# Kernel tuning notes

Measured on AMD Instinct MI355X. Metric: run time of the kernel, lower is better.

## Reference

```python
import jax, jax.numpy as jnp
import numpy as np

N = 100000        # nodes
E = 1600000       # edges (before self loops)
IN_DIM = 128
OUT_DIM = 64
HEADS = 4
CH = OUT_DIM // HEADS   # 16 channels per head
G = 64            # graphs in batch
EPS = 1e-5        # GraphNorm eps
SLOPE = 0.2       # LeakyReLU negative slope (GATv2Conv default)


def setup_inputs() -> dict:
    key = jax.random.key(0)
    ks = jax.random.split(key, 8)
    x = jax.random.normal(ks[0], (N, IN_DIM), dtype=jnp.float32)
    edge_index = jax.random.randint(ks[1], (2, E), 0, N, dtype=jnp.int64)
    batch = jnp.sort(jax.random.randint(ks[2], (N,), 0, G, dtype=jnp.int64))
    s_in = 1.0 / np.sqrt(IN_DIM)
    # GATv2Conv params (share_weights=False): W_l for source, W_r for target
    Wl = jax.random.normal(ks[3], (IN_DIM, HEADS * CH), dtype=jnp.float32) * s_in
    Wr = jax.random.normal(ks[4], (IN_DIM, HEADS * CH), dtype=jnp.float32) * s_in
    att = jax.random.normal(ks[5], (HEADS, CH), dtype=jnp.float32) * (1.0 / np.sqrt(CH))
    conv_bias = jnp.zeros((HEADS * CH,), dtype=jnp.float32)
    # skip Linear
    skip_W = jax.random.normal(ks[6], (IN_DIM, OUT_DIM), dtype=jnp.float32) * s_in
    skip_b = jax.random.normal(ks[7], (OUT_DIM,), dtype=jnp.float32) * s_in
    # GraphNorm params (PyG init: weight=1, bias=0, mean_scale=1)
    ones = jnp.ones((OUT_DIM,), dtype=jnp.float32)
    zeros = jnp.zeros((OUT_DIM,), dtype=jnp.float32)
    return {
        "x": x, "edge_index": edge_index, "batch": batch,
        "Wl": Wl, "Wr": Wr, "att": att, "conv_bias": conv_bias,
        "skip_W": skip_W, "skip_b": skip_b,
        "bn_w": ones, "bn_b": zeros, "bn_ms": ones,
        "sn_w": ones, "sn_b": zeros, "sn_ms": ones,
    }


def _gatv2(x, Wl, Wr, att, bias, src, dst):
    n = x.shape[0]
    xl = (x @ Wl).reshape(n, HEADS, CH)   # source transform (also the message)
    xr = (x @ Wr).reshape(n, HEADS, CH)   # target transform
    # GATv2: score = a . LeakyReLU(xl[j] + xr[i]) per head
    e = jax.nn.leaky_relu(xl[src] + xr[dst], SLOPE)          # [E,H,C]
    score = jnp.einsum('ehc,hc->eh', e, att)                  # [E,H]
    # segment softmax over edges sharing a target node
    smax = jax.ops.segment_max(score, dst, num_segments=n)    # [N,H]
    ex = jnp.exp(score - smax[dst])
    denom = jax.ops.segment_sum(ex, dst, num_segments=n)
    alpha = ex / denom[dst]                                   # [E,H]
    out = jax.ops.segment_sum(xl[src] * alpha[:, :, None], dst, num_segments=n)
    return out.reshape(n, HEADS * CH) + bias


def _graph_norm(x, w, b, ms, batch):
    cnt = jax.ops.segment_sum(jnp.ones((x.shape[0],), x.dtype), batch, num_segments=G)
    cnt = jnp.maximum(cnt, 1.0)[:, None]
    mean = jax.ops.segment_sum(x, batch, num_segments=G) / cnt
    cen = x - mean[batch] * ms
    var = jax.ops.segment_sum(cen * cen, batch, num_segments=G) / cnt
    inv = jax.lax.rsqrt(var + EPS)
    return w * cen * inv[batch] + b


def reference(x, edge_index, batch, Wl, Wr, att, conv_bias, skip_W, skip_b,
              bn_w, bn_b, bn_ms, sn_w, sn_b, sn_ms):
    n = x.shape[0]
    loop = jnp.arange(n, dtype=edge_index.dtype)  # add_self_loops=True default
    src = jnp.concatenate([edge_index[0], loop])
    dst = jnp.concatenate([edge_index[1], loop])
    x_main = _gatv2(x, Wl, Wr, att, conv_bias, src, dst)
    x_main = _graph_norm(x_main, bn_w, bn_b, bn_ms, batch)
    x_skip = _graph_norm(x @ skip_W + skip_b, sn_w, sn_b, sn_ms, batch)
    return jax.nn.elu(x_main + x_skip)
```

## Files before the change

kernel.cpp:

```cpp
#include <hip/hip_runtime.h>

#define IND 128
#define OUTD 64
#define NG 64
#define NPART 8
#define NSTRIPE 256
#define SLOPE 0.2f
#define EPSV 1e-5f
#define JMASK 131071
#define DEGCAP 48

typedef short bf16x8 __attribute__((ext_vector_type(8)));
typedef float f32x4 __attribute__((ext_vector_type(4)));
typedef float f32x2 __attribute__((ext_vector_type(2)));

__device__ __forceinline__ unsigned bf16rne(float f) {
  unsigned u = __float_as_uint(f);
  return (u + 0x7fffu + ((u >> 16) & 1u)) >> 16;
}
__device__ __forceinline__ unsigned pack2(float a, float b) {
  return bf16rne(a) | (bf16rne(b) << 16);
}
__device__ __forceinline__ unsigned pack2u(unsigned a, unsigned b) {
  return pack2(__uint_as_float(a), __uint_as_float(b));
}

__device__ __forceinline__ void gload_lds16(const void* g, void* l) {
  __builtin_amdgcn_global_load_lds(
      (const __attribute__((address_space(1))) void*)g,
      (__attribute__((address_space(3))) void*)l, 16, 0, 0);
}

__global__ __launch_bounds__(256) void wcvt_kernel(
    const float* __restrict__ Wl, const float* __restrict__ Wr,
    const float* __restrict__ Ws, unsigned short* __restrict__ wt) {
  int i = blockIdx.x * 256 + threadIdx.x;
  if (i >= 3 * 64 * 128) return;
  int k = i & 127, col = (i >> 7) & 63, which = i >> 13;
  const float* W = (which == 0) ? Wl : (which == 1) ? Wr : Ws;
  int row = which * 64 + col;
  int t = row >> 4, m = row & 15;
  int kc = k >> 5, quad = (k >> 3) & 3, j = k & 7;
  int slot = ((t * 4 + kc) * 4 + quad) * 16 + m;
  wt[slot * 8 + j] = (unsigned short)bf16rne(W[k * OUTD + col]);
}

__device__ __forceinline__ void gemm3_body(
    int bx, const float* __restrict__ x, const unsigned short* __restrict__ wt,
    const float* __restrict__ skip_b,
    unsigned* __restrict__ xlb, float* __restrict__ xr, float* __restrict__ xs,
    int n, uint4* ldsx) {
  int tid = threadIdx.x;
  int wave = tid >> 6, lane = tid & 63;
  int m = lane & 15, quad = lane >> 4;

#pragma unroll
  for (int i = 0; i < 8; ++i) {
    int c = i * 256 + tid;
    int row = c >> 5, u = c & 31;
    int us = u ^ (row & 7);
    int growc = min(bx * 64 + row, n - 1);
    gload_lds16(x + (size_t)growc * IND + us * 4, &ldsx[c]);
  }
  __syncthreads();

  int lbase = (wave * 16 + m) * 32;
  int swz = m & 7;
  union { uint4 u; bf16x8 v; } af[4];
#pragma unroll
  for (int kc = 0; kc < 4; ++kc) {
    int u0 = kc * 8 + quad * 2;
    uint4 A0 = ldsx[lbase + (u0 ^ swz)];
    uint4 A1 = ldsx[lbase + ((u0 + 1) ^ swz)];
    af[kc].u = make_uint4(pack2u(A0.x, A0.y), pack2u(A0.z, A0.w),
                          pack2u(A1.x, A1.y), pack2u(A1.z, A1.w));
  }

  f32x4 acc[12] = {};
#pragma unroll
  for (int kc = 0; kc < 4; ++kc) {
#pragma unroll
    for (int t = 0; t < 12; ++t) {
      const bf16x8* bp =
          (const bf16x8*)&wt[(((t * 4 + kc) * 4 + quad) * 16 + m) * 8];
      acc[t] = __builtin_amdgcn_mfma_f32_16x16x32_bf16(af[kc].v, *bp, acc[t], 0, 0, 0);
    }
  }

  float sbv[4];
#pragma unroll
  for (int q = 0; q < 4; ++q) sbv[q] = skip_b[q * 16 + m];

  int orow_base = bx * 64 + wave * 16 + quad * 4;
#pragma unroll
  for (int r = 0; r < 4; ++r) {
    int orow = orow_base + r;
    bool ok = orow < n;
#pragma unroll
    for (int t = 0; t < 4; ++t) {
      float v = acc[t][r];
      float pv = __shfl_xor(v, 1);
      if (ok && !(m & 1))
        xlb[(orow << 5) + t * 8 + (m >> 1)] = pack2(v, pv);
    }
#pragma unroll
    for (int t = 4; t < 8; ++t)
      if (ok) xr[(orow << 6) + (t - 4) * 16 + m] = acc[t][r];
#pragma unroll
    for (int t = 8; t < 12; ++t)
      if (ok) xs[(orow << 6) + (t - 8) * 16 + m] = acc[t][r] + sbv[t - 8];
  }
}

__device__ __forceinline__ void scat1(int d, int s, int lo, int hi,
                                      int* count, int* __restrict__ bucket) {
  if (d >= lo && d < hi) {
    int p = atomicAdd(&count[d], 1);
    if (p < DEGCAP) bucket[d * DEGCAP + p] = s;
  }
}

__device__ __forceinline__ void scatter_body(int r, int stripe,
                                             const int* __restrict__ src,
                                             const int* __restrict__ dst,
                                             int* count, int* __restrict__ bucket,
                                             int E, int n8) {
  int lo = r * n8, hi = lo + n8;
  int per = (((E + NSTRIPE - 1) / NSTRIPE) + 3) & ~3;
  int s0 = stripe * per;
  int s1 = min(E, s0 + per);
  for (int e = s0 + (int)threadIdx.x * 4; e < s1; e += 1024) {
    if (e + 4 <= s1) {
      int4 d4 = *(const int4*)&dst[e];
      int4 s4 = *(const int4*)&src[e];
      scat1(d4.x, s4.x, lo, hi, count, bucket);
      scat1(d4.y, s4.y, lo, hi, count, bucket);
      scat1(d4.z, s4.z, lo, hi, count, bucket);
      scat1(d4.w, s4.w, lo, hi, count, bucket);
    } else {
      for (int q = e; q < s1; ++q)
        scat1(dst[q], src[q], lo, hi, count, bucket);
    }
  }
}

__device__ __forceinline__ void goff_body(int bx, const int* __restrict__ batch,
                                          int* goff, int n) {
  int i = bx * 256 + threadIdx.x;
  if (i >= n) return;
  int b = batch[i];
  int prev = (i == 0) ? -1 : batch[i - 1];
  for (int g = prev + 1; g <= b; ++g) goff[g] = i;
  if (i == n - 1)
    for (int g = b + 1; g <= NG; ++g) goff[g] = n;
}

__global__ __launch_bounds__(256) void mega1_kernel(
    const float* __restrict__ x, const unsigned short* __restrict__ wt,
    const float* __restrict__ skip_b,
    unsigned* __restrict__ xlb, float* __restrict__ xr, float* __restrict__ xs,
    const int* __restrict__ src, const int* __restrict__ dst,
    int* count, int* bucket,
    const int* __restrict__ batch, int* goff,
    int n, int E, int n8, int nbG, int nbB, int SG, int GG) {
  __shared__ uint4 ldsx[2048];
  int group = blockIdx.x >> 3, pos = blockIdx.x & 7;
  int mn = min(SG, GG), m2 = 2 * mn;
  bool isS;
  int sub;
  if (group < m2) { isS = ((group & 1) == 0); sub = group >> 1; }
  else           { isS = (SG > GG);           sub = mn + (group - m2); }
  if (isS) {
    scatter_body(pos, sub, src, dst, count, bucket, E, n8);
  } else {
    int g = sub * 8 + pos;
    if (g < nbG) gemm3_body(g, x, wt, skip_b, xlb, xr, xs, n, ldsx);
    else if (g < nbG + nbB) goff_body(g - nbG, batch, goff, n);
  }
}

__global__ __launch_bounds__(256) void edge_kernel(
    const unsigned* __restrict__ xlb, const float* __restrict__ xr,
    const int* __restrict__ count, const int* __restrict__ bucket,
    const float* __restrict__ att, const float* __restrict__ conv_bias,
    float* __restrict__ out_main, int n) {
  int tid = threadIdx.x;
  int wave = tid >> 6;
  int lane = tid & 63;
  int half = lane >> 5;
  int sub = lane & 31;
  int bx = (int)blockIdx.x;
  int node = bx * 8 + wave * 2 + half;
  bool act = node < n;
  int nodec = min(node, n - 1);
  int base2 = (nodec << 6) | (sub << 1);

  f32x2 xrc = __builtin_nontemporal_load((const f32x2*)&xr[base2]);
  unsigned us = xlb[(nodec << 5) | sub];
  float xs0 = __uint_as_float(us << 16);
  float xs1 = __uint_as_float(us & 0xffff0000u);
  float2 att2 = *(const float2*)&att[sub << 1];

  float t0 = xs0 + xrc.x, t1 = xs1 + xrc.y;
  t0 = fmaxf(t0, SLOPE * t0);
  t1 = fmaxf(t1, SLOPE * t1);
  float s = t0 * att2.x + t1 * att2.y;
  s += __shfl_xor(s, 1);
  s += __shfl_xor(s, 2);
  s += __shfl_xor(s, 4);
  const float sself = s;

  int e0 = nodec * DEGCAP;
  int deg = min(count[nodec], DEGCAP);
  int iters = max(deg, __shfl_xor(deg, 32));

  float denom = 1.f;
  float a0 = xs0, a1 = xs1;
  int i = 0;
  for (; i + 3 < iters; i += 4) {
    float p[4], v0[4], v1[4];
#pragma unroll
    for (int k = 0; k < 4; ++k) {
      bool a = (i + k < deg);
      int e = a ? (e0 + i + k) : e0;
      int j = bucket[e] & JMASK;
      unsigned u = xlb[(j << 5) | sub];
      v0[k] = __uint_as_float(u << 16);
      v1[k] = __uint_as_float(u & 0xffff0000u);
      float tx = v0[k] + xrc.x, ty = v1[k] + xrc.y;
      tx = fmaxf(tx, SLOPE * tx); ty = fmaxf(ty, SLOPE * ty);
      float sc = tx * att2.x + ty * att2.y;
      sc += __shfl_xor(sc, 1);
      sc += __shfl_xor(sc, 2);
      sc += __shfl_xor(sc, 4);
      p[k] = a ? __expf(sc - sself) : 0.f;
    }
#pragma unroll
    for (int k = 0; k < 4; ++k) {
      denom += p[k];
      a0 += p[k] * v0[k];
      a1 += p[k] * v1[k];
    }
  }
  for (; i < iters; ++i) {
    bool a = (i < deg);
    int e = a ? (e0 + i) : e0;
    int j = bucket[e] & JMASK;
    unsigned u = xlb[(j << 5) | sub];
    float v0 = __uint_as_float(u << 16);
    float v1 = __uint_as_float(u & 0xffff0000u);
    float tx = v0 + xrc.x, ty = v1 + xrc.y;
    tx = fmaxf(tx, SLOPE * tx); ty = fmaxf(ty, SLOPE * ty);
    float sc = tx * att2.x + ty * att2.y;
    sc += __shfl_xor(sc, 1);
    sc += __shfl_xor(sc, 2);
    sc += __shfl_xor(sc, 4);
    float p = a ? __expf(sc - sself) : 0.f;
    denom += p;
    a0 += p * v0;
    a1 += p * v1;
  }
  float inv = 1.f / denom;
  float2 cb = *(const float2*)&conv_bias[sub << 1];
  if (act) {
    f32x2 o; o.x = a0 * inv + cb.x; o.y = a1 * inv + cb.y;
    __builtin_nontemporal_store(o, (f32x2*)&out_main[base2]);
  }
}

__global__ __launch_bounds__(256) void stats_part_kernel(
    const float* __restrict__ mainv, const float* __restrict__ xs,
    const int* __restrict__ goff, float* __restrict__ part) {
  int g = blockIdx.x, q = blockIdx.y;
  int start = goff[g], end = goff[g + 1];
  int col = threadIdx.x & 63, grp = threadIdx.x >> 6;
  float s1m = 0.f, s2m = 0.f, s1s = 0.f, s2s = 0.f;
  for (int node = start + q * 4 + grp; node < end; node += 4 * NPART) {
    float vm = __builtin_nontemporal_load(&mainv[(node << 6) | col]);
    float vs = __builtin_nontemporal_load(&xs[(node << 6) | col]);
    s1m += vm; s2m += vm * vm;
    s1s += vs; s2s += vs * vs;
  }
  __shared__ float red[4][4][64];
  red[0][grp][col] = s1m; red[1][grp][col] = s2m;
  red[2][grp][col] = s1s; red[3][grp][col] = s2s;
  __syncthreads();
  if (threadIdx.x < 64) {
    int c = threadIdx.x;
    float* dst = &part[(g * NPART + q) * 256];
#pragma unroll
    for (int st = 0; st < 4; ++st) {
      float s = red[st][0][c] + red[st][1][c] + red[st][2][c] + red[st][3][c];
      dst[st * 64 + c] = s;
    }
  }
}

__global__ void stats_comb_kernel(
    const float* __restrict__ part, const int* __restrict__ goff,
    const float* __restrict__ bn_w, const float* __restrict__ bn_b,
    const float* __restrict__ bn_ms,
    const float* __restrict__ sn_w, const float* __restrict__ sn_b,
    const float* __restrict__ sn_ms,
    float* __restrict__ Am, float* __restrict__ Bm,
    float* __restrict__ As, float* __restrict__ Bs) {
  int g = blockIdx.x;
  int c = threadIdx.x;
  float S1m = 0.f, S2m = 0.f, S1s = 0.f, S2s = 0.f;
  for (int q = 0; q < NPART; ++q) {
    const float* p = &part[(g * NPART + q) * 256];
    S1m += p[c];       S2m += p[64 + c];
    S1s += p[128 + c]; S2s += p[192 + c];
  }
  float cnt = fmaxf((float)(goff[g + 1] - goff[g]), 1.f);
  float meanM = S1m / cnt;
  float aM = meanM * bn_ms[c];
  float varM = S2m / cnt - 2.f * aM * meanM + aM * aM;
  float invM = rsqrtf(varM + EPSV);
  float am = bn_w[c] * invM;
  Am[g * OUTD + c] = am;
  Bm[g * OUTD + c] = bn_b[c] - am * aM;
  float meanS = S1s / cnt;
  float aS = meanS * sn_ms[c];
  float varS = S2s / cnt - 2.f * aS * meanS + aS * aS;
  float invS = rsqrtf(varS + EPSV);
  float as_ = sn_w[c] * invS;
  As[g * OUTD + c] = as_;
  Bs[g * OUTD + c] = sn_b[c] - as_ * aS;
}

__global__ __launch_bounds__(256) void final_kernel(
    const float* __restrict__ xs, const int* __restrict__ batch,
    const float* __restrict__ Am, const float* __restrict__ Bm,
    const float* __restrict__ As, const float* __restrict__ Bs,
    float* out, int n) {
  int idx = blockIdx.x * 256 + threadIdx.x;
  if (idx >= n * 16) return;
  int node = idx >> 4;
  int c4 = (idx & 15) << 2;
  int g = batch[node];
  f32x4 mv = __builtin_nontemporal_load((const f32x4*)&out[idx << 2]);
  f32x4 sv = __builtin_nontemporal_load((const f32x4*)&xs[idx << 2]);
  f32x4 A1 = *(const f32x4*)&Am[g * OUTD + c4];
  f32x4 B1 = *(const f32x4*)&Bm[g * OUTD + c4];
  f32x4 A2 = *(const f32x4*)&As[g * OUTD + c4];
  f32x4 B2 = *(const f32x4*)&Bs[g * OUTD + c4];
  f32x4 v;
  v.x = A1.x * mv.x + B1.x + A2.x * sv.x + B2.x;
  v.y = A1.y * mv.y + B1.y + A2.y * sv.y + B2.y;
  v.z = A1.z * mv.z + B1.z + A2.z * sv.z + B2.z;
  v.w = A1.w * mv.w + B1.w + A2.w * sv.w + B2.w;
  v.x = (v.x > 0.f) ? v.x : (__expf(v.x) - 1.f);
  v.y = (v.y > 0.f) ? v.y : (__expf(v.y) - 1.f);
  v.z = (v.z > 0.f) ? v.z : (__expf(v.z) - 1.f);
  v.w = (v.w > 0.f) ? v.w : (__expf(v.w) - 1.f);
  __builtin_nontemporal_store(v, (f32x4*)&out[idx << 2]);
}

extern "C" void kernel_launch(void* const* d_in, const int* in_sizes, int n_in,
                              void* d_out, int out_size, void* d_ws, size_t ws_size,
                              hipStream_t stream) {
  const float* x        = (const float*)d_in[0];
  const int*   ei       = (const int*)d_in[1];
  const int*   batch    = (const int*)d_in[2];
  const float* Wl       = (const float*)d_in[3];
  const float* Wr       = (const float*)d_in[4];
  const float* att      = (const float*)d_in[5];
  const float* conv_b   = (const float*)d_in[6];
  const float* skip_W   = (const float*)d_in[7];
  const float* skip_b   = (const float*)d_in[8];
  const float* bn_w     = (const float*)d_in[9];
  const float* bn_b     = (const float*)d_in[10];
  const float* bn_ms    = (const float*)d_in[11];
  const float* sn_w     = (const float*)d_in[12];
  const float* sn_b     = (const float*)d_in[13];
  const float* sn_ms    = (const float*)d_in[14];

  int n = in_sizes[0] / IND;
  int E = in_sizes[1] / 2;
  const int* src = ei;
  const int* dst = ei + E;
  float* out = (float*)d_out;

  char* w = (char*)d_ws;
  int* count  = (int*)w;   w += (size_t)(n + 64) * 4;
  int* goff   = (int*)w;   w += (size_t)(NG + 64) * 4;
  float* Am   = (float*)w; w += (size_t)NG * OUTD * 4;
  float* Bm   = (float*)w; w += (size_t)NG * OUTD * 4;
  float* As   = (float*)w; w += (size_t)NG * OUTD * 4;
  float* Bs   = (float*)w; w += (size_t)NG * OUTD * 4;
  float* part = (float*)w; w += (size_t)NG * NPART * 256 * 4;
  unsigned short* wt = (unsigned short*)w; w += (size_t)3 * 64 * IND * 2;
  int* bucket = (int*)w;   w += (size_t)n * DEGCAP * 4;
  unsigned* xlb = (unsigned*)w; w += (size_t)n * 32 * 4;
  float* xr   = (float*)w; w += (size_t)n * OUTD * 4;
  float* xs   = (float*)w; w += (size_t)n * OUTD * 4;

  int n8 = (n + 7) / 8;
  int nbG = (n + 63) / 64;
  int nbB = (n + 255) / 256;
  int SG = NSTRIPE;
  int GG = (nbG + nbB + 7) / 8;

  (void)hipMemsetAsync(count, 0, (size_t)(n + 1) * 4, stream);

  wcvt_kernel<<<(3 * 64 * IND + 255) / 256, 256, 0, stream>>>(Wl, Wr, skip_W, wt);

  mega1_kernel<<<8 * (SG + GG), 256, 0, stream>>>(
      x, wt, skip_b, xlb, xr, xs, src, dst, count, bucket, batch, goff,
      n, E, n8, nbG, nbB, SG, GG);

  edge_kernel<<<(n + 7) / 8, 256, 0, stream>>>(xlb, xr, count, bucket, att, conv_b,
                                               out, n);
  dim3 sg(NG, NPART);
  stats_part_kernel<<<sg, 256, 0, stream>>>(out, xs, goff, part);
  stats_comb_kernel<<<NG, 64, 0, stream>>>(part, goff, bn_w, bn_b, bn_ms,
                                           sn_w, sn_b, sn_ms, Am, Bm, As, Bs);
  final_kernel<<<(n * 16 + 255) / 256, 256, 0, stream>>>(xs, batch, Am, Bm, As, Bs,
                                                         out, n);
}
```

Baseline: 326.2 us.

## Fuse GraphNorm main-branch statistics into edge kernel via per-block atomics

The edge kernel now reduces sum and sum-of-squares of its output per graph in shared memory and atomically adds them into a per-graph accumulator. The stats pass then only reads the skip branch, so it no longer re-reads the 25.6 MB main output. The cost is an extra __syncthreads, LDS traffic and about 12.5k blocks each issuing 128 float atomics per distinct graph. Because sorted batches make graphs contiguous, most blocks hit a single graph, which concentrates atomic contention on the same addresses.

```diff
diff --git a/kernel.cpp b/kernel.cpp
--- a/kernel.cpp
+++ b/kernel.cpp
@@ -183,6 +183,7 @@
     const unsigned* __restrict__ xlb, const float* __restrict__ xr,
     const int* __restrict__ count, const int* __restrict__ bucket,
     const float* __restrict__ att, const float* __restrict__ conv_bias,
+    const int* __restrict__ batch, float* __restrict__ Sm,
     float* __restrict__ out_main, int n) {
   int tid = threadIdx.x;
   int wave = tid >> 6;
@@ -262,34 +263,59 @@
   }
   float inv = 1.f / denom;
   float2 cb = *(const float2*)&conv_bias[sub << 1];
+  float o0 = act ? (a0 * inv + cb.x) : 0.f;
+  float o1 = act ? (a1 * inv + cb.y) : 0.f;
   if (act) {
-    f32x2 o; o.x = a0 * inv + cb.x; o.y = a1 * inv + cb.y;
+    f32x2 o; o.x = o0; o.y = o1;
     __builtin_nontemporal_store(o, (f32x2*)&out_main[base2]);
   }
+
+  __shared__ float sv[8][64];
+  __shared__ float sq[8][64];
+  __shared__ int gidv[8];
+  int slot = wave * 2 + half;
+  sv[slot][2 * sub]     = o0;
+  sv[slot][2 * sub + 1] = o1;
+  sq[slot][2 * sub]     = o0 * o0;
+  sq[slot][2 * sub + 1] = o1 * o1;
+  if (sub == 0) gidv[slot] = act ? batch[nodec] : -1;
+  __syncthreads();
+  if (tid < 64) {
+    int col = tid;
+    for (int s2 = 0; s2 < 8; ++s2) {
+      int g = gidv[s2];
+      if (g < 0) continue;
+      bool dup = false;
+      for (int t2 = 0; t2 < s2; ++t2) dup |= (gidv[t2] == g);
+      if (dup) continue;
+      float s1v = 0.f, s1q = 0.f;
+      for (int t2 = s2; t2 < 8; ++t2)
+        if (gidv[t2] == g) { s1v += sv[t2][col]; s1q += sq[t2][col]; }
+      atomicAdd(&Sm[g * 128 + col], s1v);
+      atomicAdd(&Sm[g * 128 + 64 + col], s1q);
+    }
+  }
 }
 
 __global__ __launch_bounds__(256) void stats_part_kernel(
-    const float* __restrict__ mainv, const float* __restrict__ xs,
+    const float* __restrict__ xs,
     const int* __restrict__ goff, float* __restrict__ part) {
   int g = blockIdx.x, q = blockIdx.y;
   int start = goff[g], end = goff[g + 1];
   int col = threadIdx.x & 63, grp = threadIdx.x >> 6;
-  float s1m = 0.f, s2m = 0.f, s1s = 0.f, s2s = 0.f;
+  float s1s = 0.f, s2s = 0.f;
   for (int node = start + q * 4 + grp; node < end; node += 4 * NPART) {
-    float vm = __builtin_nontemporal_load(&mainv[(node << 6) | col]);
     float vs = __builtin_nontemporal_load(&xs[(node << 6) | col]);
-    s1m += vm; s2m += vm * vm;
     s1s += vs; s2s += vs * vs;
   }
-  __shared__ float red[4][4][64];
-  red[0][grp][col] = s1m; red[1][grp][col] = s2m;
-  red[2][grp][col] = s1s; red[3][grp][col] = s2s;
+  __shared__ float red[2][4][64];
+  red[0][grp][col] = s1s; red[1][grp][col] = s2s;
   __syncthreads();
   if (threadIdx.x < 64) {
     int c = threadIdx.x;
-    float* dst = &part[(g * NPART + q) * 256];
-#pragma unroll
-    for (int st = 0; st < 4; ++st) {
+    float* dst = &part[(g * NPART + q) * 128];
+#pragma unroll
+    for (int st = 0; st < 2; ++st) {
       float s = red[st][0][c] + red[st][1][c] + red[st][2][c] + red[st][3][c];
       dst[st * 64 + c] = s;
     }
@@ -297,7 +323,8 @@
 }
 
 __global__ void stats_comb_kernel(
-    const float* __restrict__ part, const int* __restrict__ goff,
+    const float* __restrict__ part, const float* __restrict__ Sm,
+    const int* __restrict__ goff,
     const float* __restrict__ bn_w, const float* __restrict__ bn_b,
     const float* __restrict__ bn_ms,
     const float* __restrict__ sn_w, const float* __restrict__ sn_b,
@@ -306,11 +333,12 @@
     float* __restrict__ As, float* __restrict__ Bs) {
   int g = blockIdx.x;
   int c = threadIdx.x;
-  float S1m = 0.f, S2m = 0.f, S1s = 0.f, S2s = 0.f;
+  float S1m = Sm[g * 128 + c];
+  float S2m = Sm[g * 128 + 64 + c];
+  float S1s = 0.f, S2s = 0.f;
   for (int q = 0; q < NPART; ++q) {
-    const float* p = &part[(g * NPART + q) * 256];
-    S1m += p[c];       S2m += p[64 + c];
-    S1s += p[128 + c]; S2s += p[192 + c];
+    const float* p = &part[(g * NPART + q) * 128];
+    S1s += p[c];  S2s += p[64 + c];
   }
   float cnt = fmaxf((float)(goff[g + 1] - goff[g]), 1.f);
   float meanM = S1m / cnt;
@@ -384,12 +412,13 @@
 
   char* w = (char*)d_ws;
   int* count  = (int*)w;   w += (size_t)(n + 64) * 4;
+  float* Sm   = (float*)w; w += (size_t)NG * 128 * 4;
   int* goff   = (int*)w;   w += (size_t)(NG + 64) * 4;
   float* Am   = (float*)w; w += (size_t)NG * OUTD * 4;
   float* Bm   = (float*)w; w += (size_t)NG * OUTD * 4;
   float* As   = (float*)w; w += (size_t)NG * OUTD * 4;
   float* Bs   = (float*)w; w += (size_t)NG * OUTD * 4;
-  float* part = (float*)w; w += (size_t)NG * NPART * 256 * 4;
+  float* part = (float*)w; w += (size_t)NG * NPART * 128 * 4;
   unsigned short* wt = (unsigned short*)w; w += (size_t)3 * 64 * IND * 2;
   int* bucket = (int*)w;   w += (size_t)n * DEGCAP * 4;
   unsigned* xlb = (unsigned*)w; w += (size_t)n * 32 * 4;
@@ -402,7 +431,8 @@
   int SG = NSTRIPE;
   int GG = (nbG + nbB + 7) / 8;
 
-  (void)hipMemsetAsync(count, 0, (size_t)(n + 1) * 4, stream);
+  (void)hipMemsetAsync(count, 0, (size_t)(n + 64) * 4 + (size_t)NG * 128 * 4,
+                       stream);
 
   wcvt_kernel<<<(3 * 64 * IND + 255) / 256, 256, 0, stream>>>(Wl, Wr, skip_W, wt);
 
@@ -411,10 +441,10 @@
       n, E, n8, nbG, nbB, SG, GG);
 
   edge_kernel<<<(n + 7) / 8, 256, 0, stream>>>(xlb, xr, count, bucket, att, conv_b,
-                                               out, n);
+                                               batch, Sm, out, n);
   dim3 sg(NG, NPART);
-  stats_part_kernel<<<sg, 256, 0, stream>>>(out, xs, goff, part);
-  stats_comb_kernel<<<NG, 64, 0, stream>>>(part, goff, bn_w, bn_b, bn_ms,
+  stats_part_kernel<<<sg, 256, 0, stream>>>(xs, goff, part);
+  stats_comb_kernel<<<NG, 64, 0, stream>>>(part, Sm, goff, bn_w, bn_b, bn_ms,
                                            sn_w, sn_b, sn_ms, Am, Bm, As, Bs);
   final_kernel<<<(n * 16 + 255) / 256, 256, 0, stream>>>(xs, batch, Am, Bm, As, Bs,
                                                          out, n);
```

Measured after the change: 332.7 us. +2.0%, slower.
